# Kernel tuning notes

Hardware: AMD Instinct MI355X
Metric: run time of the kernel (lower is better)

## Reference

```python
import jax, jax.numpy as jnp
import numpy as np

NUM_GROUPS = 32
EPS = 1e-5


def group_norm(x, w, b):
    # x: [B, C, H, W]
    B, C, H, W = x.shape
    g = x.reshape(B, NUM_GROUPS, C // NUM_GROUPS, H, W)
    mu = g.mean(axis=(2, 3, 4), keepdims=True)
    var = g.var(axis=(2, 3, 4), keepdims=True)
    g = (g - mu) * jax.lax.rsqrt(var + EPS)
    x = g.reshape(B, C, H, W)
    return x * w[None, :, None, None] + b[None, :, None, None]


def conv1x1(x, w, b):
    # 1x1 conv == channel matmul; x: [B, C, H, W], w: [O, C], b: [O]
    return jnp.einsum('bchw,oc->bohw', x, w) + b[None, :, None, None]


def setup_inputs() -> dict:
    key = jax.random.key(0)
    ks = jax.random.split(key, 11)
    C = 512
    B, H, W = 4, 64, 64
    s = 1.0 / np.sqrt(C)
    return {
        'x': jax.random.normal(ks[0], (B, C, H, W), jnp.float32),
        'gn_w': jax.random.uniform(ks[1], (C,), jnp.float32, 0.5, 1.5),
        'gn_b': jax.random.normal(ks[2], (C,), jnp.float32) * 0.1,
        'wq': jax.random.normal(ks[3], (C, C), jnp.float32) * s,
        'bq': jax.random.normal(ks[4], (C,), jnp.float32) * 0.01,
        'wk': jax.random.normal(ks[5], (C, C), jnp.float32) * s,
        'bk': jax.random.normal(ks[6], (C,), jnp.float32) * 0.01,
        'wv': jax.random.normal(ks[7], (C, C), jnp.float32) * s,
        'bv': jax.random.normal(ks[8], (C,), jnp.float32) * 0.01,
        'wo': jax.random.normal(ks[9], (C, C), jnp.float32) * s,
        'bo': jax.random.normal(ks[10], (C,), jnp.float32) * 0.01,
    }


def reference(x, gn_w, gn_b, wq, bq, wk, bk, wv, bv, wo, bo):
    B, C, H, W = x.shape
    h_ = group_norm(x, gn_w, gn_b)
    q = conv1x1(h_, wq, bq).reshape(B, C, H * W)   # [B, C, HW]
    k = conv1x1(h_, wk, bk).reshape(B, C, H * W)
    v = conv1x1(h_, wv, bv).reshape(B, C, H * W)
    # scores: q^T k, scaled by C^-0.5; softmax over keys
    scores = jnp.einsum('bci,bcj->bij', q, k) * (C ** -0.5)  # [B, HW, HW]
    attn = jax.nn.softmax(scores, axis=-1)
    # h_[b,c,i] = sum_j v[b,c,j] * attn[b,i,j]
    h_ = jnp.einsum('bcj,bij->bci', v, attn).reshape(B, C, H, W)
    return x + conv1x1(h_, wo, bo)
```

## Files before the change

kernel.cpp:

```cpp
#include <hip/hip_runtime.h>
#include <hip/hip_bf16.h>

typedef __attribute__((ext_vector_type(8))) __bf16 bf16x8;
typedef __attribute__((ext_vector_type(4))) float f32x4;

__device__ __forceinline__ unsigned short f2bf(float f) {
  union { float f; unsigned u; } v; v.f = f;
  unsigned r = v.u + 0x7fffu + ((v.u >> 16) & 1u);
  return (unsigned short)(r >> 16);
}

__device__ __forceinline__ void gload_lds16(const void* g, void* s) {
  __builtin_amdgcn_global_load_lds(
      (const __attribute__((address_space(1))) void*)g,
      (__attribute__((address_space(3))) void*)s, 16, 0, 0);
}

__global__ __launch_bounds__(256) void convert_w(
    const float* __restrict__ wq, const float* __restrict__ wk,
    const float* __restrict__ wv, const float* __restrict__ wo,
    unsigned short* __restrict__ dst) {
  const int m = blockIdx.x >> 10;
  const float* src = (m == 0) ? wq : (m == 1) ? wk : (m == 2) ? wv : wo;
  const int idx = ((blockIdx.x & 1023) << 8) | threadIdx.x;
  dst[m * 262144 + idx] = f2bf(src[idx]);
}

__global__ __launch_bounds__(256) void zero_k(float* __restrict__ p, int n) {
  const int i = blockIdx.x * 256 + threadIdx.x;
  if (i < n) p[i] = 0.f;
}

__global__ __launch_bounds__(256) void gn_stats(
    const float* __restrict__ x, float2* __restrict__ partials) {
  const int bg = blockIdx.x >> 2, part = blockIdx.x & 3;
  const float* xg = x + (size_t)bg * 65536 + part * 1024;
  const int t = threadIdx.x;
  float s = 0.f, ss = 0.f;
#pragma unroll
  for (int r = 0; r < 16; ++r) {
    const float4 v = *(const float4*)(xg + (size_t)r * 4096 + t * 4);
    s += v.x + v.y + v.z + v.w;
    ss += v.x * v.x + v.y * v.y + v.z * v.z + v.w * v.w;
  }
#pragma unroll
  for (int m = 32; m; m >>= 1) { s += __shfl_xor(s, m); ss += __shfl_xor(ss, m); }
  __shared__ float red[8];
  const int wave = t >> 6, lane = t & 63;
  if (lane == 0) { red[wave] = s; red[wave + 4] = ss; }
  __syncthreads();
  if (t == 0) {
    float2 p;
    p.x = red[0] + red[1] + red[2] + red[3];
    p.y = red[4] + red[5] + red[6] + red[7];
    partials[blockIdx.x] = p;
  }
}

__global__ __launch_bounds__(256) void gn_apply(
    const float* __restrict__ x, const float2* __restrict__ partials,
    const float* __restrict__ gw, const float* __restrict__ gb,
    unsigned short* __restrict__ h_t) {
  const int bg = blockIdx.x >> 3, cc = blockIdx.x & 7;
  const int b = bg >> 5, g = bg & 31;
  const int t = threadIdx.x;
  __shared__ float chs[32];
  __shared__ unsigned short tile[16][520];
  if (t < 16) {
    const float2 p0 = partials[bg * 4 + 0], p1 = partials[bg * 4 + 1];
    const float2 p2 = partials[bg * 4 + 2], p3 = partials[bg * 4 + 3];
    const float S = p0.x + p1.x + p2.x + p3.x;
    const float SS = p0.y + p1.y + p2.y + p3.y;
    const float mu = S * (1.f / 65536.f);
    const float rstd = rsqrtf(SS * (1.f / 65536.f) - mu * mu + 1e-5f);
    const float sc = gw[g * 16 + t] * rstd;
    chs[t] = sc;
    chs[16 + t] = gb[g * 16 + t] - mu * sc;
  }
  __syncthreads();
  const float* xg = x + (size_t)bg * 65536 + cc * 512;
#pragma unroll
  for (int rr = 0; rr < 8; ++rr) {
    const int r = rr * 2 + (t >> 7), i = (t & 127) * 4;
    const float4 v = *(const float4*)(xg + (size_t)r * 4096 + i);
    const float sc = chs[r], sh = chs[16 + r];
    ushort4 o;
    o.x = f2bf(v.x * sc + sh); o.y = f2bf(v.y * sc + sh);
    o.z = f2bf(v.z * sc + sh); o.w = f2bf(v.w * sc + sh);
    *(ushort4*)&tile[r][i] = o;
  }
  __syncthreads();
  unsigned short* outp = h_t + ((size_t)b * 4096 + cc * 512) * 512 + g * 16;
#pragma unroll
  for (int rep = 0; rep < 4; ++rep) {
    const int task = rep * 256 + t;
    const int nl = task >> 1, half = (task & 1) * 8;
    ushort4 o0, o1;
    o0.x = tile[half + 0][nl]; o0.y = tile[half + 1][nl];
    o0.z = tile[half + 2][nl]; o0.w = tile[half + 3][nl];
    o1.x = tile[half + 4][nl]; o1.y = tile[half + 5][nl];
    o1.z = tile[half + 6][nl]; o1.w = tile[half + 7][nl];
    *(ushort4*)(outp + (size_t)nl * 512 + half) = o0;
    *(ushort4*)(outp + (size_t)nl * 512 + half + 4) = o1;
  }
}

__global__ __launch_bounds__(256) void reduce4_k(
    const float* __restrict__ part, const float* __restrict__ l,
    unsigned short* __restrict__ dst) {
  const size_t i = ((size_t)blockIdx.x * 256 + threadIdx.x) * 4;
  f32x4 s0 = *(const f32x4*)(part + i);
  f32x4 s1 = *(const f32x4*)(part + 2097152 + i);
  f32x4 s2 = *(const f32x4*)(part + 4194304 + i);
  f32x4 s3 = *(const f32x4*)(part + 6291456 + i);
  f32x4 s = (s0 + s1) + (s2 + s3);
  const float inv = 1.f / l[i >> 9];
  ushort4 o;
  o.x = f2bf(s[0] * inv); o.y = f2bf(s[1] * inv);
  o.z = f2bf(s[2] * inv); o.w = f2bf(s[3] * inv);
  *(ushort4*)(dst + i) = o;
}

__global__ __launch_bounds__(512, 4) void gemm_s256(
    const unsigned short* __restrict__ A, const unsigned short* __restrict__ Bt,
    unsigned short* __restrict__ Out, float* __restrict__ lsum) {
  __shared__ __align__(16) char smem[73728];
  const int tid = threadIdx.x;
  const int wave = tid >> 6, lane = tid & 63;
  const int l15 = lane & 15, l4 = lane >> 4;
  const int wm = wave >> 1, wn = wave & 1;

  const int id = blockIdx.y * 32 + blockIdx.x;
  const int xcd = id & 7, j = id >> 3;
  const int by = ((xcd >> 1) << 2) + (j >> 4);
  const int bx = ((xcd & 1) << 4) + (j & 15);
  const int row0 = by << 8, col0 = bx << 7;

  const int ar = tid >> 2;
  const int akc = (tid & 3) ^ ((tid >> 4) & 3);

  auto stage = [&](int kt, int bi) {
    const int kb = kt << 5;
    char* base = smem + bi * 24576;
    const unsigned short* gA = A + (size_t)(row0 + ar) * 512 + kb + akc * 8;
    const unsigned short* gB = Bt + (size_t)(col0 + ar) * 512 + kb + akc * 8;
    gload_lds16(gA, base + wave * 1024);
    gload_lds16(gA + (size_t)128 * 512, base + 8192 + wave * 1024);
    gload_lds16(gB, base + 16384 + wave * 1024);
  };

  f32x4 acc[4][4];
#pragma unroll
  for (int r = 0; r < 4; ++r)
#pragma unroll
    for (int c = 0; c < 4; ++c) acc[r][c] = (f32x4)0.f;

  const int xsw = (l4 ^ (l15 >> 2)) << 4;

  auto compute = [&](int bi) {
    const char* pa = smem + bi * 24576 + (wm * 64 + l15) * 64 + xsw;
    const char* pb = smem + bi * 24576 + 16384 + (wn * 64 + l15) * 64 + xsw;
    bf16x8 af[4], bfr[4];
#pragma unroll
    for (int r = 0; r < 4; ++r) af[r] = *(const bf16x8*)(pa + r * 1024);
#pragma unroll
    for (int c = 0; c < 4; ++c) bfr[c] = *(const bf16x8*)(pb + c * 1024);
#pragma unroll
    for (int r = 0; r < 4; ++r)
#pragma unroll
      for (int c = 0; c < 4; ++c)
        acc[r][c] = __builtin_amdgcn_mfma_f32_16x16x32_bf16(af[r], bfr[c], acc[r][c], 0, 0, 0);
  };

  stage(0, 0);
  stage(1, 1);
  int bi = 0;
  for (int kt = 0; kt < 15; ++kt) {
    asm volatile("s_waitcnt vmcnt(3)" ::: "memory");
    __builtin_amdgcn_s_barrier();
    __builtin_amdgcn_sched_barrier(0);
    if (kt + 2 < 16) stage(kt + 2, (kt + 2) % 3);
    compute(bi);
    bi = (bi == 2) ? 0 : bi + 1;
  }
  asm volatile("s_waitcnt vmcnt(0)" ::: "memory");
  __builtin_amdgcn_s_barrier();
  __builtin_amdgcn_sched_barrier(0);
  compute(bi);

  __syncthreads();
  unsigned short* tile = (unsigned short*)smem;
#pragma unroll
  for (int p = 0; p < 2; ++p) {
    if ((wm >> 1) == p) {
#pragma unroll
      for (int c = 0; c < 4; ++c) {
        const int coll = wn * 64 + c * 16 + l15;
#pragma unroll
        for (int r = 0; r < 4; ++r) {
          const int rowl = (wm & 1) * 64 + r * 16 + l4 * 4;
#pragma unroll
          for (int j = 0; j < 4; ++j)
            tile[(rowl + j) * 136 + coll] = f2bf(__expf(acc[r][c][j]));
        }
      }
    }
    __syncthreads();
#pragma unroll
    for (int it = 0; it < 4; ++it) {
      const int idx = it * 512 + tid;
      const int rw = idx >> 4, ch = (idx & 15) * 8;
      const uint4 vv = *(const uint4*)&tile[rw * 136 + ch];
      *(uint4*)(Out + (size_t)(row0 + p * 128 + rw) * 4096 + col0 + ch) = vv;
      const unsigned* uu = (const unsigned*)&vv;
      float s = 0.f;
#pragma unroll
      for (int q = 0; q < 4; ++q) {
        union { unsigned u; float f; } w;
        w.u = uu[q] << 16; s += w.f;
        w.u = uu[q] & 0xffff0000u; s += w.f;
      }
      s += __shfl_xor(s, 1); s += __shfl_xor(s, 2);
      s += __shfl_xor(s, 4); s += __shfl_xor(s, 8);
      if ((lane & 15) == 0) atomicAdd(&lsum[row0 + p * 128 + rw], s);
    }
    __syncthreads();
  }
}

template <bool OUT_BF16, int BIAS_MODE, bool RESID, bool TRANS_OUT, int SWZ,
          bool COAL>
__global__ __launch_bounds__(256) void gemm_bt(
    const unsigned short* __restrict__ A, long long sA, int lda,
    const unsigned short* __restrict__ Bt, long long sB, int ldb,
    void* __restrict__ OutV, long long sO, int ldo,
    const float* __restrict__ bias,
    const float* __restrict__ resid, long long sR,
    int K, float scale) {
  __shared__ __align__(16) char smem[49152];
  const int tid = threadIdx.x;
  const int wave = tid >> 6, lane = tid & 63;
  const int l15 = lane & 15, l4 = lane >> 4;
  const int wm = wave >> 1, wn = wave & 1;

  int bx = blockIdx.x, by = blockIdx.y, bz = blockIdx.z;
  if constexpr (SWZ == 1) {
    const int id = by * 32 + bx;
    const int xcd = id & 7, j = id >> 3;
    by = ((xcd >> 1) << 3) + (j >> 4);
    bx = ((xcd & 1) << 4) + (j & 15);
  } else if constexpr (SWZ == 2) {
    const int L = bx + ((by + (bz << 5)) << 2);
    const int xcd = L & 7, j = L >> 3;
    const int pair = xcd * 16 + (j >> 2);
    bx = j & 3;
    by = pair & 31;
    bz = pair >> 5;
  }
  const int row0 = by << 7, col0 = bx << 7;
  A += (size_t)bz * sA;
  Bt += (size_t)bz * sB;
  if (RESID) resid += (size_t)bz * sR;
  if constexpr (BIAS_MODE == 3) bias += (size_t)bz * sR;
  char* outB = (char*)OutV + (size_t)bz * sO * (OUT_BF16 ? 2 : 4);

  const int ar = tid >> 2;
  const int akc = (tid & 3) ^ ((tid >> 4) & 3);

  auto stage = [&](int kt, int bi) {
    const int kb = kt << 5;
    char* sAl = smem + bi * 16384 + wave * 1024;
    char* sBl = sAl + 8192;
    const unsigned short* gA = A + (size_t)(row0 + ar) * lda + kb + akc * 8;
    const unsigned short* gB = Bt + (size_t)(col0 + ar) * ldb + kb + akc * 8;
    gload_lds16(gA, sAl);
    gload_lds16(gB, sBl);
    gload_lds16(gA + (size_t)64 * lda, sAl + 4096);
    gload_lds16(gB + (size_t)64 * ldb, sBl + 4096);
  };

  f32x4 acc[4][4];
#pragma unroll
  for (int r = 0; r < 4; ++r)
#pragma unroll
    for (int c = 0; c < 4; ++c) acc[r][c] = (f32x4)0.f;

  const int nk = K >> 5;
  const int xsw = (l4 ^ (l15 >> 2)) << 4;

  auto compute = [&](int bi) {
    const char* pa = smem + bi * 16384 + (wm * 64 + l15) * 64 + xsw;
    const char* pb = smem + bi * 16384 + 8192 + (wn * 64 + l15) * 64 + xsw;
    bf16x8 af[4], bfr[4];
#pragma unroll
    for (int r = 0; r < 4; ++r) af[r] = *(const bf16x8*)(pa + r * 1024);
#pragma unroll
    for (int c = 0; c < 4; ++c) bfr[c] = *(const bf16x8*)(pb + c * 1024);
#pragma unroll
    for (int r = 0; r < 4; ++r)
#pragma unroll
      for (int c = 0; c < 4; ++c)
        acc[r][c] = __builtin_amdgcn_mfma_f32_16x16x32_bf16(af[r], bfr[c], acc[r][c], 0, 0, 0);
  };

  stage(0, 0);
  stage(1, 1);
  int bi = 0;
  for (int kt = 0; kt < nk - 1; ++kt) {
    asm volatile("s_waitcnt vmcnt(4)" ::: "memory");
    __builtin_amdgcn_s_barrier();
    __builtin_amdgcn_sched_barrier(0);
    if (kt + 2 < nk) stage(kt + 2, (kt + 2) % 3);
    compute(bi);
    bi = (bi == 2) ? 0 : bi + 1;
  }
  asm volatile("s_waitcnt vmcnt(0)" ::: "memory");
  __builtin_amdgcn_s_barrier();
  __builtin_amdgcn_sched_barrier(0);
  compute(bi);

  if constexpr (COAL && !TRANS_OUT) {
    __syncthreads();
    if constexpr (OUT_BF16) {
      unsigned short* tile = (unsigned short*)smem;
#pragma unroll
      for (int c = 0; c < 4; ++c) {
        const int coll = wn * 64 + c * 16 + l15;
        float badd = 0.f;
        if constexpr (BIAS_MODE == 1) badd = bias[col0 + coll];
#pragma unroll
        for (int r = 0; r < 4; ++r) {
          const int rowl = wm * 64 + r * 16 + l4 * 4;
#pragma unroll
          for (int j = 0; j < 4; ++j) {
            float v;
            if constexpr (BIAS_MODE == 3)
              v = acc[r][c][j] * (1.0f / bias[row0 + rowl + j]);
            else
              v = (acc[r][c][j] + badd) * scale;
            tile[(rowl + j) * 136 + coll] = f2bf(v);
          }
        }
      }
      __syncthreads();
      unsigned short* outp = (unsigned short*)outB;
#pragma unroll
      for (int it = 0; it < 8; ++it) {
        const int idx = it * 256 + tid;
        const int rw = idx >> 4, ch = (idx & 15) * 8;
        const uint4 vv = *(const uint4*)&tile[rw * 136 + ch];
        *(uint4*)(outp + (size_t)(row0 + rw) * ldo + col0 + ch) = vv;
      }
    } else {
      float* tile = (float*)smem;
#pragma unroll
      for (int p = 0; p < 2; ++p) {
        if (wm == p) {
#pragma unroll
          for (int c = 0; c < 4; ++c) {
            const int coll = wn * 64 + c * 16 + l15;
            float badd = 0.f;
            if constexpr (BIAS_MODE == 1) badd = bias[col0 + coll];
#pragma unroll
            for (int r = 0; r < 4; ++r) {
              const int rowl = r * 16 + l4 * 4;
#pragma unroll
              for (int j = 0; j < 4; ++j) {
                float v = acc[r][c][j] + badd;
                if constexpr (BIAS_MODE == 2) v += bias[row0 + p * 64 + rowl + j];
                tile[(rowl + j) * 132 + coll] = v * scale;
              }
            }
          }
        }
        __syncthreads();
        float* outp = (float*)outB;
#pragma unroll
        for (int it = 0; it < 8; ++it) {
          const int idx = it * 256 + tid;
          const int rw = idx >> 5, ch = (idx & 31) * 4;
          const int rowg = row0 + p * 64 + rw;
          f32x4 v = *(const f32x4*)&tile[rw * 132 + ch];
          if constexpr (RESID) {
            const float* rp = resid + (size_t)rowg * ldo + col0 + ch;
            v[0] += rp[0]; v[1] += rp[1]; v[2] += rp[2]; v[3] += rp[3];
          }
          *(f32x4*)(outp + (size_t)rowg * ldo + col0 + ch) = v;
        }
        __syncthreads();
      }
    }
  } else if constexpr (!TRANS_OUT) {
#pragma unroll
    for (int c = 0; c < 4; ++c) {
      const int colg = col0 + wn * 64 + c * 16 + l15;
      float badd = 0.f;
      if constexpr (BIAS_MODE == 1) badd = bias[colg];
#pragma unroll
      for (int r = 0; r < 4; ++r) {
        const int rowg = row0 + wm * 64 + r * 16 + l4 * 4;
#pragma unroll
        for (int j = 0; j < 4; ++j) {
          float v = acc[r][c][j] + badd;
          if constexpr (BIAS_MODE == 2) v += bias[rowg + j];
          v *= scale;
          if constexpr (RESID) v += resid[(size_t)(rowg + j) * ldo + colg];
          if constexpr (OUT_BF16)
            ((unsigned short*)outB)[(size_t)(rowg + j) * ldo + colg] = f2bf(v);
          else
            ((float*)outB)[(size_t)(rowg + j) * ldo + colg] = v;
        }
      }
    }
  } else {
    __syncthreads();
    unsigned short* tile = (unsigned short*)smem;
#pragma unroll
    for (int c = 0; c < 4; ++c) {
      const int coll = wn * 64 + c * 16 + l15;
      float badd = 0.f;
      if constexpr (BIAS_MODE == 1) badd = bias[col0 + coll];
#pragma unroll
      for (int r = 0; r < 4; ++r) {
        const int rowl = wm * 64 + r * 16 + l4 * 4;
#pragma unroll
        for (int j = 0; j < 4; ++j)
          tile[(rowl + j) * 132 + coll] = f2bf((acc[r][c][j] + badd) * scale);
      }
    }
    __syncthreads();
    unsigned short* outp = (unsigned short*)outB;
#pragma unroll 8
    for (int it = 0; it < 64; ++it) {
      const int idx = it * 256 + tid;
      const int cl = idx >> 7, il = idx & 127;
      outp[(size_t)(col0 + cl) * ldo + row0 + il] = tile[il * 132 + cl];
    }
  }
}

extern "C" void kernel_launch(void* const* d_in, const int* in_sizes, int n_in,
                              void* d_out, int out_size, void* d_ws, size_t ws_size,
                              hipStream_t stream) {
  const float* x   = (const float*)d_in[0];
  const float* gnw = (const float*)d_in[1];
  const float* gnb = (const float*)d_in[2];
  const float* wq  = (const float*)d_in[3];
  const float* bq  = (const float*)d_in[4];
  const float* wk  = (const float*)d_in[5];
  const float* bk  = (const float*)d_in[6];
  const float* wv  = (const float*)d_in[7];
  const float* bv  = (const float*)d_in[8];
  const float* wo  = (const float*)d_in[9];
  const float* bo  = (const float*)d_in[10];
  float* out = (float*)d_out;
  char* ws = (char*)d_ws;

  const size_t MB = 1u << 20;
  float2*         gnp  = (float2*)ws;
  float*          lrow = (float*)(ws + 64 * 1024);
  unsigned short* wbf  = (unsigned short*)(ws + 1 * MB);
  unsigned short* h_t  = (unsigned short*)(ws + 3 * MB);
  unsigned short* q_t  = (unsigned short*)(ws + 19 * MB);
  unsigned short* k_t  = (unsigned short*)(ws + 35 * MB);
  unsigned short* v_ct = (unsigned short*)(ws + 51 * MB);
  unsigned short* h2_t = (unsigned short*)(ws + 67 * MB);
  unsigned short* Pbuf = (unsigned short*)(ws + 83 * MB);
  float*          part = (float*)(ws + 115 * MB);

  const long long BS = 2097152;
  const long long PBS = 16777216;
  const float qscale = 0.044194173824159216f;
  const bool batched = ws_size >= 212 * MB;

  convert_w<<<dim3(4096), dim3(256), 0, stream>>>(wq, wk, wv, wo, wbf);
  gn_stats<<<dim3(512), dim3(256), 0, stream>>>(x, gnp);
  gn_apply<<<dim3(1024), dim3(256), 0, stream>>>(x, gnp, gnw, gnb, h_t);

  gemm_bt<true, 1, false, false, 0, true><<<dim3(4, 32, 4), 256, 0, stream>>>(
      h_t, BS, 512, wbf + 0, 0, 512, q_t, BS, 512, bq, nullptr, 0, 512, qscale);
  gemm_bt<true, 1, false, false, 0, true><<<dim3(4, 32, 4), 256, 0, stream>>>(
      h_t, BS, 512, wbf + 262144, 0, 512, k_t, BS, 512, bk, nullptr, 0, 512, 1.0f);
  gemm_bt<true, 1, false, true, 0, false><<<dim3(4, 32, 4), 256, 0, stream>>>(
      h_t, BS, 512, wbf + 524288, 0, 512, v_ct, BS, 4096, bv, nullptr, 0, 512, 1.0f);

  if (batched) {
    zero_k<<<dim3(64), dim3(256), 0, stream>>>(lrow, 16384);
    for (int b = 0; b < 4; ++b)
      gemm_s256<<<dim3(32, 16), dim3(512), 0, stream>>>(
          q_t + (size_t)b * BS, k_t + (size_t)b * BS,
          Pbuf + (size_t)b * PBS, lrow + b * 4096);
    gemm_bt<true, 3, false, false, 2, true><<<dim3(4, 32, 4), 256, 0, stream>>>(
        Pbuf, PBS, 4096, v_ct, BS, 4096,
        h2_t, BS, 512, lrow, nullptr, 4096, 4096, 1.0f);
  } else {
    for (int b = 0; b < 4; ++b) {
      zero_k<<<dim3(16), dim3(256), 0, stream>>>(lrow, 4096);
      gemm_s256<<<dim3(32, 16), dim3(512), 0, stream>>>(
          q_t + (size_t)b * BS, k_t + (size_t)b * BS, Pbuf, lrow);
      gemm_bt<false, 0, false, false, 0, true><<<dim3(4, 32, 4), 256, 0, stream>>>(
          Pbuf, 1024, 4096, v_ct + (size_t)b * BS, 1024, 4096,
          part, 2097152, 512, nullptr, nullptr, 0, 1024, 1.0f);
      reduce4_k<<<dim3(2048), dim3(256), 0, stream>>>(part, lrow, h2_t + (size_t)b * BS);
    }
  }

  gemm_bt<false, 2, true, false, 0, true><<<dim3(32, 4, 4), 256, 0, stream>>>(
      wbf + 786432, 0, 512, h2_t, BS, 512, out, BS, 4096, bo, x, BS, 512, 1.0f);
}
```

Before: 302.6 us.

## Batch score GEMM over z and add dedicated 256x128 triple-buffered PV GEMM

The score GEMM is launched once with a batch grid dimension instead of four per-batch launches, which removes launch gaps and tail effects. The P·V product gets its own kernel with 512 threads, a 256x128 tile, K-step 64 and a three-stage LDS pipeline (144KB shared memory). That kernel interleaves MFMA phases with async global-to-LDS loads and remaps blocks across XCDs for L2 locality. The larger LDS footprint limits occupancy, and the hand-written waitcnt/barrier schedule is fragile.

After: 272.1 us. 1.11x faster.

```diff
diff --git a/kernel.cpp b/kernel.cpp
--- a/kernel.cpp
+++ b/kernel.cpp
@@ -130,6 +130,12 @@
   const int l15 = lane & 15, l4 = lane >> 4;
   const int wm = wave >> 1, wn = wave & 1;
 
+  const int bz = blockIdx.z;
+  A += (size_t)bz * 2097152;
+  Bt += (size_t)bz * 2097152;
+  Out += (size_t)bz * 16777216;
+  lsum += (size_t)bz * 4096;
+
   const int id = blockIdx.y * 32 + blockIdx.x;
   const int xcd = id & 7, j = id >> 3;
   const int by = ((xcd >> 1) << 2) + (j >> 4);
@@ -225,6 +231,159 @@
       if ((lane & 15) == 0) atomicAdd(&lsum[row0 + p * 128 + rw], s);
     }
     __syncthreads();
+  }
+}
+
+__global__ __launch_bounds__(512, 2) void gemm_pv(
+    const unsigned short* __restrict__ P, const unsigned short* __restrict__ Vt,
+    unsigned short* __restrict__ Out, const float* __restrict__ lrow) {
+  __shared__ __align__(16) char smem[147456];
+  const int tid = threadIdx.x;
+  const int wave = tid >> 6, lane = tid & 63;
+  const int l15 = lane & 15, l4 = lane >> 4;
+  const int wm = wave >> 1, wn = wave & 1;
+
+  const int L = blockIdx.x + ((blockIdx.y + (blockIdx.z << 4)) << 2);
+  const int xcd = L & 7, j = L >> 3;
+  const int panel = xcd * 8 + (j >> 2);
+  const int bx = j & 3, by = panel & 15, bz = panel >> 4;
+  const int row0 = by << 8, col0 = bx << 7;
+  P += (size_t)bz * 16777216;
+  Vt += (size_t)bz * 2097152;
+  Out += (size_t)bz * 2097152;
+  lrow += bz * 4096;
+
+  const int sr = tid >> 3;
+  const int sc8 = (tid & 7) ^ (sr & 7);
+  const unsigned short* gA = P + (size_t)(row0 + sr) * 4096 + sc8 * 8;
+  const unsigned short* gB = Vt + (size_t)(col0 + sr) * 4096 + sc8 * 8;
+
+  auto stA = [&](int kt, int bi, int p) {
+    gload_lds16(gA + (size_t)(p << 6) * 4096 + (kt << 6),
+                smem + bi * 49152 + p * 8192 + wave * 1024);
+  };
+  auto stB = [&](int kt, int bi, int p) {
+    gload_lds16(gB + (size_t)(p << 6) * 4096 + (kt << 6),
+                smem + bi * 49152 + 32768 + p * 8192 + wave * 1024);
+  };
+
+  f32x4 acc[4][4];
+#pragma unroll
+  for (int r = 0; r < 4; ++r)
+#pragma unroll
+    for (int c = 0; c < 4; ++c) acc[r][c] = (f32x4)0.f;
+
+  const int sw0 = (l4 ^ (l15 & 7)) << 4;
+  const int sw1 = ((4 + l4) ^ (l15 & 7)) << 4;
+  const int arow = (wm * 64 + l15) << 7;
+  const int brow = (wn * 64 + l15) << 7;
+
+  bf16x8 bfr[4][2];
+
+  stA(0, 0, 0); stA(0, 0, 1); stA(0, 0, 2); stA(0, 0, 3);
+  stB(0, 0, 0); stB(0, 0, 1);
+  stA(1, 1, 0); stA(1, 1, 1); stA(1, 1, 2); stA(1, 1, 3);
+  stB(1, 1, 0); stB(1, 1, 1);
+  asm volatile("s_waitcnt vmcnt(6)" ::: "memory");
+  __builtin_amdgcn_s_barrier();
+  __builtin_amdgcn_sched_barrier(0);
+
+  int bi = 0;
+#pragma unroll 1
+  for (int kt = 0; kt < 64; ++kt) {
+    const char* bufA = smem + bi * 49152;
+    const char* bufB = bufA + 32768;
+    const int pb = (bi + 2) % 3;
+    const bool pre = (kt + 2 < 64);
+    bf16x8 a0, a1;
+    a0 = *(const bf16x8*)(bufA + arow + sw0);
+    a1 = *(const bf16x8*)(bufA + arow + sw1);
+#pragma unroll
+    for (int c = 0; c < 4; ++c) {
+      bfr[c][0] = *(const bf16x8*)(bufB + brow + c * 2048 + sw0);
+      bfr[c][1] = *(const bf16x8*)(bufB + brow + c * 2048 + sw1);
+    }
+    if (pre) { stA(kt + 2, pb, 0); stA(kt + 2, pb, 1); }
+    __builtin_amdgcn_s_barrier();
+    asm volatile("s_waitcnt lgkmcnt(0)" ::: "memory");
+    __builtin_amdgcn_sched_barrier(0);
+    __builtin_amdgcn_s_setprio(1);
+#pragma unroll
+    for (int c = 0; c < 4; ++c) {
+      acc[0][c] = __builtin_amdgcn_mfma_f32_16x16x32_bf16(a0, bfr[c][0], acc[0][c], 0, 0, 0);
+      acc[0][c] = __builtin_amdgcn_mfma_f32_16x16x32_bf16(a1, bfr[c][1], acc[0][c], 0, 0, 0);
+    }
+    __builtin_amdgcn_s_setprio(0);
+    __builtin_amdgcn_s_barrier();
+    a0 = *(const bf16x8*)(bufA + arow + 2048 + sw0);
+    a1 = *(const bf16x8*)(bufA + arow + 2048 + sw1);
+    if (pre) { stA(kt + 2, pb, 2); stA(kt + 2, pb, 3); }
+    __builtin_amdgcn_s_barrier();
+    asm volatile("s_waitcnt lgkmcnt(0)" ::: "memory");
+    __builtin_amdgcn_sched_barrier(0);
+    __builtin_amdgcn_s_setprio(1);
+#pragma unroll
+    for (int c = 0; c < 4; ++c) {
+      acc[1][c] = __builtin_amdgcn_mfma_f32_16x16x32_bf16(a0, bfr[c][0], acc[1][c], 0, 0, 0);
+      acc[1][c] = __builtin_amdgcn_mfma_f32_16x16x32_bf16(a1, bfr[c][1], acc[1][c], 0, 0, 0);
+    }
+    __builtin_amdgcn_s_setprio(0);
+    __builtin_amdgcn_s_barrier();
+    a0 = *(const bf16x8*)(bufA + arow + 4096 + sw0);
+    a1 = *(const bf16x8*)(bufA + arow + 4096 + sw1);
+    if (pre) { stB(kt + 2, pb, 0); stB(kt + 2, pb, 1); }
+    __builtin_amdgcn_s_barrier();
+    asm volatile("s_waitcnt lgkmcnt(0)" ::: "memory");
+    __builtin_amdgcn_sched_barrier(0);
+    __builtin_amdgcn_s_setprio(1);
+#pragma unroll
+    for (int c = 0; c < 4; ++c) {
+      acc[2][c] = __builtin_amdgcn_mfma_f32_16x16x32_bf16(a0, bfr[c][0], acc[2][c], 0, 0, 0);
+      acc[2][c] = __builtin_amdgcn_mfma_f32_16x16x32_bf16(a1, bfr[c][1], acc[2][c], 0, 0, 0);
+    }
+    __builtin_amdgcn_s_setprio(0);
+    __builtin_amdgcn_s_barrier();
+    a0 = *(const bf16x8*)(bufA + arow + 6144 + sw0);
+    a1 = *(const bf16x8*)(bufA + arow + 6144 + sw1);
+    __builtin_amdgcn_s_barrier();
+    asm volatile("s_waitcnt lgkmcnt(0)" ::: "memory");
+    __builtin_amdgcn_sched_barrier(0);
+    __builtin_amdgcn_s_setprio(1);
+#pragma unroll
+    for (int c = 0; c < 4; ++c) {
+      acc[3][c] = __builtin_amdgcn_mfma_f32_16x16x32_bf16(a0, bfr[c][0], acc[3][c], 0, 0, 0);
+      acc[3][c] = __builtin_amdgcn_mfma_f32_16x16x32_bf16(a1, bfr[c][1], acc[3][c], 0, 0, 0);
+    }
+    __builtin_amdgcn_s_setprio(0);
+    if (pre) asm volatile("s_waitcnt vmcnt(6)" ::: "memory");
+    else     asm volatile("s_waitcnt vmcnt(0)" ::: "memory");
+    __builtin_amdgcn_s_barrier();
+    __builtin_amdgcn_sched_barrier(0);
+    bi = (bi == 2) ? 0 : bi + 1;
+  }
+
+  __syncthreads();
+  unsigned short* tile = (unsigned short*)smem;
+#pragma unroll
+  for (int c = 0; c < 4; ++c) {
+    const int coll = wn * 64 + c * 16 + l15;
+#pragma unroll
+    for (int r = 0; r < 4; ++r) {
+      const int rowl = wm * 64 + r * 16 + l4 * 4;
+#pragma unroll
+      for (int j = 0; j < 4; ++j) {
+        const float v = acc[r][c][j] * (1.0f / lrow[row0 + rowl + j]);
+        tile[(rowl + j) * 136 + coll] = f2bf(v);
+      }
+    }
+  }
+  __syncthreads();
+#pragma unroll
+  for (int it = 0; it < 8; ++it) {
+    const int idx = it * 512 + tid;
+    const int rw = idx >> 4, ch = (idx & 15) * 8;
+    const uint4 vv = *(const uint4*)&tile[rw * 136 + ch];
+    *(uint4*)(Out + (size_t)(row0 + rw) * 512 + col0 + ch) = vv;
   }
 }
 
@@ -486,13 +645,8 @@
 
   if (batched) {
     zero_k<<<dim3(64), dim3(256), 0, stream>>>(lrow, 16384);
-    for (int b = 0; b < 4; ++b)
-      gemm_s256<<<dim3(32, 16), dim3(512), 0, stream>>>(
-          q_t + (size_t)b * BS, k_t + (size_t)b * BS,
-          Pbuf + (size_t)b * PBS, lrow + b * 4096);
-    gemm_bt<true, 3, false, false, 2, true><<<dim3(4, 32, 4), 256, 0, stream>>>(
-        Pbuf, PBS, 4096, v_ct, BS, 4096,
-        h2_t, BS, 512, lrow, nullptr, 4096, 4096, 1.0f);
+    gemm_s256<<<dim3(32, 16, 4), dim3(512), 0, stream>>>(q_t, k_t, Pbuf, lrow);
+    gemm_pv<<<dim3(4, 16, 4), dim3(512), 0, stream>>>(Pbuf, v_ct, h2_t, lrow);
   } else {
     for (int b = 0; b < 4; ++b) {
       zero_k<<<dim3(16), dim3(256), 0, stream>>>(lrow, 4096);
```
